# Kernel optimization log

Hardware: AMD Instinct MI355X
Metric: run time of the kernel (lower is better)

Reference implementation:

```python
import jax, jax.numpy as jnp
import numpy as np

N_NODES = 50000
N_EDGES = 800000
IN_CH = 128
HEADS = 4
OUT_CH = 32


def setup_inputs() -> dict:
    key = jax.random.key(0)
    k1, k2, k3, k4 = jax.random.split(key, 4)
    x = jax.random.normal(k1, (N_NODES, IN_CH), dtype=jnp.float32)
    edge_index = jax.random.randint(k2, (2, N_EDGES), 0, N_NODES, dtype=jnp.int64)
    # nn.Linear weight [out, in] with xavier-uniform init
    limW = float(np.sqrt(6.0 / (IN_CH + HEADS * OUT_CH)))
    W = jax.random.uniform(k3, (HEADS * OUT_CH, IN_CH), minval=-limW, maxval=limW, dtype=jnp.float32)
    lima = float(np.sqrt(6.0 / (HEADS + 2 * OUT_CH)))
    att = jax.random.uniform(k4, (HEADS, 2 * OUT_CH), minval=-lima, maxval=lima, dtype=jnp.float32)
    bias = jnp.zeros((HEADS * OUT_CH,), dtype=jnp.float32)
    return {"x": x, "edge_index": edge_index, "W": W, "att": att, "bias": bias}


def reference(x, edge_index, W, att, bias):
    n = x.shape[0]
    heads, two_c = att.shape
    out_ch = two_c // 2
    loop = jnp.arange(n, dtype=edge_index.dtype)
    src = jnp.concatenate([edge_index[0], loop])  # [E+n]
    dst = jnp.concatenate([edge_index[1], loop])  # [E+n]
    h = (x @ W.T).reshape(n, heads, out_ch)       # [n, H, C]
    h_src = h[src]                                # [E+n, H, C]
    h_dst = h[dst]                                # [E+n, H, C]
    # e = sum over channels of att applied to [h_src || h_dst]
    e = (jnp.einsum('ehc,hc->eh', h_src, att[:, :out_ch])
         + jnp.einsum('ehc,hc->eh', h_dst, att[:, out_ch:]))  # [E+n, H]
    e = jax.nn.leaky_relu(e, negative_slope=0.2)
    # segment softmax over incoming edges per dst node
    e_max = jax.ops.segment_max(e, dst, num_segments=n)        # [n, H]
    alpha = jnp.exp(e - e_max[dst])                            # [E+n, H]
    a_sum = jax.ops.segment_sum(alpha, dst, num_segments=n)    # [n, H]
    alpha = alpha / jnp.maximum(a_sum[dst], 1e-10)
    weighted = h_src * alpha[..., None]                        # [E+n, H, C]
    out = jax.ops.segment_sum(weighted, dst, num_segments=n)   # [n, H, C]
    out = out.reshape(n, heads * out_ch)                       # concat=True
    return out + bias
```

## Files before the change

### kernel.cpp

```cpp
#include <hip/hip_runtime.h>
#include <hip/hip_bf16.h>
#include <math.h>

#define N_NODES 50000
#define N_EDGES 800000
#define IN_CH   128
#define HEADS   4
#define OUT_CH  32
#define HC      128
#define WROWS   136

#define CB_SHIFT 7
#define CB_NODES 128
#define N_CB     391
#define NBK      128
#define EPB      (N_EDGES / NBK)
#define PCAP     44
#define ND_CAP   48
#define CB_CAP   2560

#define NG_TOT   782
#define NG_A     586
#define NG_B     (NG_TOT - NG_A)

typedef __attribute__((ext_vector_type(8))) short short8;
typedef __attribute__((ext_vector_type(4))) float floatx4;

__device__ __forceinline__ short f2bf(float f) {
    __hip_bfloat16 h = __float2bfloat16(f);
    return *reinterpret_cast<short*>(&h);
}

__device__ __forceinline__ void gemm_role(
    short* __restrict__ Wlds, int node_base,
    const float* __restrict__ x, const float* __restrict__ W,
    const float* __restrict__ att, __hip_bfloat16* __restrict__ hbuf,
    float* __restrict__ asrc, float* __restrict__ adst) {

    const int tid  = threadIdx.x;
    const int wave = tid >> 6;
    const int lane = tid & 63;
    const int col  = lane & 15;
    const int q    = lane >> 4;

    {
        int row  = tid >> 1;
        int half = tid & 1;
        const float4* Wr = (const float4*)(W + row * IN_CH + half * 64);
        short* dp = Wlds + row * WROWS + half * 64;
#pragma unroll
        for (int i = 0; i < 16; ++i) {
            float4 v = Wr[i];
            ushort4 p;
            p.x = (unsigned short)f2bf(v.x);
            p.y = (unsigned short)f2bf(v.y);
            p.z = (unsigned short)f2bf(v.z);
            p.w = (unsigned short)f2bf(v.w);
            *(ushort4*)(dp + i * 4) = p;
        }
    }

    float attS[8], attD[8];
#pragma unroll
    for (int t = 0; t < 8; ++t) {
        int base = (t >> 1) * 64 + (t & 1) * 16 + col;
        attS[t] = att[base];
        attD[t] = att[base + 32];
    }

    __syncthreads();

    const int node0 = node_base + wave * 16;
    const int m  = node0 + col;
    const int mc = min(m, N_NODES - 1);

    floatx4 acc[8];
#pragma unroll
    for (int t = 0; t < 8; ++t) acc[t] = (floatx4){0.f, 0.f, 0.f, 0.f};

#pragma unroll
    for (int ks = 0; ks < 4; ++ks) {
        const float4* xp = (const float4*)(x + (size_t)mc * IN_CH + ks * 32 + q * 8);
        float4 v0 = xp[0];
        float4 v1 = xp[1];
        short8 af;
        af[0] = f2bf(v0.x); af[1] = f2bf(v0.y); af[2] = f2bf(v0.z); af[3] = f2bf(v0.w);
        af[4] = f2bf(v1.x); af[5] = f2bf(v1.y); af[6] = f2bf(v1.z); af[7] = f2bf(v1.w);
#pragma unroll
        for (int t = 0; t < 8; ++t) {
            const short8 bf = *(const short8*)(Wlds + (t * 16 + col) * WROWS + ks * 32 + q * 8);
            acc[t] = __builtin_amdgcn_mfma_f32_16x16x32_bf16(af, bf, acc[t], 0, 0, 0);
        }
    }

#pragma unroll
    for (int r = 0; r < 4; ++r) {
        const int node = node0 + q * 4 + r;
        const bool valid = node < N_NODES;
        float hs[4] = {0.f, 0.f, 0.f, 0.f};
        float hd[4] = {0.f, 0.f, 0.f, 0.f};
#pragma unroll
        for (int t = 0; t < 8; ++t) {
            float v = acc[t][r];
            if (valid) hbuf[(size_t)node * HC + t * 16 + col] = __float2bfloat16(v);
            hs[t >> 1] = fmaf(v, attS[t], hs[t >> 1]);
            hd[t >> 1] = fmaf(v, attD[t], hd[t >> 1]);
        }
#pragma unroll
        for (int off = 8; off; off >>= 1) {
#pragma unroll
            for (int h = 0; h < 4; ++h) {
                hs[h] += __shfl_down(hs[h], off, 16);
                hd[h] += __shfl_down(hd[h], off, 16);
            }
        }
        if (col == 0 && valid) {
#pragma unroll
            for (int h = 0; h < 4; ++h) {
                asrc[node * HEADS + h] = hs[h];
                adst[node * HEADS + h] = hd[h];
            }
        }
    }
}

__global__ __launch_bounds__(256) void kA_fused(
    const int* __restrict__ src, const int* __restrict__ dst,
    unsigned* __restrict__ priv, int* __restrict__ cnt2,
    const float* __restrict__ x, const float* __restrict__ W,
    const float* __restrict__ att, __hip_bfloat16* __restrict__ hbuf,
    float* __restrict__ asrc, float* __restrict__ adst) {

    __shared__ short smem[128 * WROWS];
    const int tid = threadIdx.x;

    if (blockIdx.x < NBK) {
        int* lcnt = (int*)smem;
        const int blk = blockIdx.x;
        for (int i = tid; i < N_CB; i += 256) lcnt[i] = 0;
        __syncthreads();

        const int e0 = blk * EPB;
        for (int e = e0 + tid; e < e0 + EPB; e += 256) {
            int s = src[e];
            int d = dst[e];
            int cb = d >> CB_SHIFT;
            int pos = atomicAdd(&lcnt[cb], 1);
            if (pos < PCAP)
                priv[((size_t)cb * NBK + blk) * PCAP + pos] =
                    ((unsigned)(d & (CB_NODES - 1)) << 16) | (unsigned)s;
        }
        __syncthreads();
        for (int i = tid; i < N_CB; i += 256)
            cnt2[blk * N_CB + i] = min(lcnt[i], PCAP);
        return;
    }

    gemm_role(smem, (blockIdx.x - NBK) * 64, x, W, att, hbuf, asrc, adst);
}

__global__ __launch_bounds__(256) void kB_fused(
    const int* __restrict__ cnt2, const unsigned* __restrict__ priv,
    unsigned short* __restrict__ csr16, unsigned* __restrict__ meta,
    const float* __restrict__ x, const float* __restrict__ W,
    const float* __restrict__ att, __hip_bfloat16* __restrict__ hbuf,
    float* __restrict__ asrc, float* __restrict__ adst) {

    __shared__ short smem[128 * WROWS];
    const int tid = threadIdx.x;

    if (blockIdx.x >= N_CB) {
        gemm_role(smem, (NG_A + (int)blockIdx.x - N_CB) * 64, x, W, att, hbuf, asrc, adst);
        return;
    }

    unsigned short* list = (unsigned short*)smem;
    int* lcnt  = (int*)(smem + 6400);
    int* ccnt  = (int*)(smem + 6656);
    int* lpre  = (int*)(smem + 6912);
    int* lcnt2 = (int*)(smem + 7168);

    const int b = blockIdx.x;
    const int node0 = b << CB_SHIFT;
    const int nInB  = min(CB_NODES, N_NODES - node0);

    if (tid < CB_NODES) lcnt[tid] = 0;
    if (tid < NBK) lcnt2[tid] = cnt2[tid * N_CB + b];
    __syncthreads();

    const unsigned* p = priv + (size_t)b * NBK * PCAP;
    for (int idx = tid; idx < NBK * PCAP; idx += 256) {
        int blk = (idx * 5958) >> 18;
        int j   = idx - blk * PCAP;
        if (j < lcnt2[blk]) {
            unsigned ent = p[idx];
            int dl   = ent >> 16;
            int slot = atomicAdd(&lcnt[dl], 1);
            if (slot < ND_CAP) list[dl * ND_CAP + slot] = (unsigned short)(ent & 0xFFFFu);
        }
    }
    __syncthreads();

    if (tid < CB_NODES) { ccnt[tid] = min(lcnt[tid], ND_CAP); lpre[tid] = ccnt[tid]; }
    __syncthreads();
    for (int d = 1; d < CB_NODES; d <<= 1) {
        int v = (tid >= d && tid < CB_NODES) ? lpre[tid - d] : 0;
        __syncthreads();
        if (tid < CB_NODES) lpre[tid] += v;
        __syncthreads();
    }

    if (tid < nInB) {
        int cnt  = ccnt[tid];
        int excl = lpre[tid] - cnt;
        meta[node0 + tid] = (unsigned)(b * CB_CAP + excl) | ((unsigned)cnt << 24);
    }

    const int total = lpre[CB_NODES - 1];
    __syncthreads();
    for (int idx = tid; idx < total; idx += 256) {
        int n = 0;
#pragma unroll
        for (int s = 64; s; s >>= 1)
            if (idx >= lpre[n + s - 1]) n += s;
        int j = idx - (lpre[n] - ccnt[n]);
        csr16[b * CB_CAP + idx] = list[n * ND_CAP + j];
    }
}

__device__ __forceinline__ float edge_w(float t) {
    t = fmaxf(t, 0.2f * t);
    return __expf(t);
}

__global__ __launch_bounds__(256) void kb6_agg(
    const unsigned* __restrict__ meta, const unsigned short* __restrict__ csr16,
    const unsigned* __restrict__ hb, const float* __restrict__ asrc,
    const float* __restrict__ adst, const float* __restrict__ bias,
    float* __restrict__ out) {

    const int node = __builtin_amdgcn_readfirstlane(blockIdx.x * 4 + (threadIdx.x >> 6));
    if (node >= N_NODES) return;
    const int lane = threadIdx.x & 63;
    const int h    = lane >> 4;

    const unsigned mt = meta[node];
    const int cnt = (int)(mt >> 24);
    const unsigned short* p = csr16 + (mt & 0xFFFFFFu);

    const float ad = adst[node * HEADS + h];

    unsigned us = hb[node * 64 + lane];
    float wS = edge_w(asrc[node * HEADS + h] + ad);
    float ds = wS;
    float ax = wS * __uint_as_float(us << 16);
    float ay = wS * __uint_as_float(us & 0xffff0000u);

    int e = 0;
    for (; e + 7 < cnt; e += 8) {
        int s0 = p[e],     s1 = p[e + 1], s2 = p[e + 2], s3 = p[e + 3];
        int s4 = p[e + 4], s5 = p[e + 5], s6 = p[e + 6], s7 = p[e + 7];
        unsigned u0 = hb[s0 * 64 + lane];
        unsigned u1 = hb[s1 * 64 + lane];
        unsigned u2 = hb[s2 * 64 + lane];
        unsigned u3 = hb[s3 * 64 + lane];
        unsigned u4 = hb[s4 * 64 + lane];
        unsigned u5 = hb[s5 * 64 + lane];
        unsigned u6 = hb[s6 * 64 + lane];
        unsigned u7 = hb[s7 * 64 + lane];
        float w0 = edge_w(asrc[s0 * HEADS + h] + ad);
        float w1 = edge_w(asrc[s1 * HEADS + h] + ad);
        float w2 = edge_w(asrc[s2 * HEADS + h] + ad);
        float w3 = edge_w(asrc[s3 * HEADS + h] + ad);
        float w4 = edge_w(asrc[s4 * HEADS + h] + ad);
        float w5 = edge_w(asrc[s5 * HEADS + h] + ad);
        float w6 = edge_w(asrc[s6 * HEADS + h] + ad);
        float w7 = edge_w(asrc[s7 * HEADS + h] + ad);
        ds += ((w0 + w1) + (w2 + w3)) + ((w4 + w5) + (w6 + w7));
        ax = fmaf(w0, __uint_as_float(u0 << 16), ax);
        ay = fmaf(w0, __uint_as_float(u0 & 0xffff0000u), ay);
        ax = fmaf(w1, __uint_as_float(u1 << 16), ax);
        ay = fmaf(w1, __uint_as_float(u1 & 0xffff0000u), ay);
        ax = fmaf(w2, __uint_as_float(u2 << 16), ax);
        ay = fmaf(w2, __uint_as_float(u2 & 0xffff0000u), ay);
        ax = fmaf(w3, __uint_as_float(u3 << 16), ax);
        ay = fmaf(w3, __uint_as_float(u3 & 0xffff0000u), ay);
        ax = fmaf(w4, __uint_as_float(u4 << 16), ax);
        ay = fmaf(w4, __uint_as_float(u4 & 0xffff0000u), ay);
        ax = fmaf(w5, __uint_as_float(u5 << 16), ax);
        ay = fmaf(w5, __uint_as_float(u5 & 0xffff0000u), ay);
        ax = fmaf(w6, __uint_as_float(u6 << 16), ax);
        ay = fmaf(w6, __uint_as_float(u6 & 0xffff0000u), ay);
        ax = fmaf(w7, __uint_as_float(u7 << 16), ax);
        ay = fmaf(w7, __uint_as_float(u7 & 0xffff0000u), ay);
    }
    for (; e + 3 < cnt; e += 4) {
        int s0 = p[e], s1 = p[e + 1], s2 = p[e + 2], s3 = p[e + 3];
        unsigned u0 = hb[s0 * 64 + lane];
        unsigned u1 = hb[s1 * 64 + lane];
        unsigned u2 = hb[s2 * 64 + lane];
        unsigned u3 = hb[s3 * 64 + lane];
        float w0 = edge_w(asrc[s0 * HEADS + h] + ad);
        float w1 = edge_w(asrc[s1 * HEADS + h] + ad);
        float w2 = edge_w(asrc[s2 * HEADS + h] + ad);
        float w3 = edge_w(asrc[s3 * HEADS + h] + ad);
        ds += (w0 + w1) + (w2 + w3);
        ax = fmaf(w0, __uint_as_float(u0 << 16), ax);
        ay = fmaf(w0, __uint_as_float(u0 & 0xffff0000u), ay);
        ax = fmaf(w1, __uint_as_float(u1 << 16), ax);
        ay = fmaf(w1, __uint_as_float(u1 & 0xffff0000u), ay);
        ax = fmaf(w2, __uint_as_float(u2 << 16), ax);
        ay = fmaf(w2, __uint_as_float(u2 & 0xffff0000u), ay);
        ax = fmaf(w3, __uint_as_float(u3 << 16), ax);
        ay = fmaf(w3, __uint_as_float(u3 & 0xffff0000u), ay);
    }
    for (; e < cnt; ++e) {
        int s0 = p[e];
        unsigned u0 = hb[s0 * 64 + lane];
        float w0 = edge_w(asrc[s0 * HEADS + h] + ad);
        ds += w0;
        ax = fmaf(w0, __uint_as_float(u0 << 16), ax);
        ay = fmaf(w0, __uint_as_float(u0 & 0xffff0000u), ay);
    }

    float inv = 1.0f / fmaxf(ds, 1e-10f);
    float2 b = *(const float2*)(bias + lane * 2);
    float2 o;
    o.x = ax * inv + b.x;
    o.y = ay * inv + b.y;
    *(float2*)(out + (size_t)node * HC + lane * 2) = o;
}

extern "C" void kernel_launch(void* const* d_in, const int* in_sizes, int n_in,
                              void* d_out, int out_size, void* d_ws, size_t ws_size,
                              hipStream_t stream) {
    const float* x    = (const float*)d_in[0];
    const int*   ei   = (const int*)d_in[1];
    const float* W    = (const float*)d_in[2];
    const float* att  = (const float*)d_in[3];
    const float* bias = (const float*)d_in[4];
    float* out = (float*)d_out;

    const int* src = ei;
    const int* dst = ei + N_EDGES;

    char* ws = (char*)d_ws;
    __hip_bfloat16* hbuf = (__hip_bfloat16*)ws;
    float*    asrc = (float*)(ws + 12800000);
    float*    adst = (float*)(ws + 13600000);
    unsigned* priv = (unsigned*)(ws + 14400000);
    int*      cnt2 = (int*)(ws + 23208448);
    unsigned* meta = (unsigned*)(ws + 23408640);
    unsigned short* csr16 = (unsigned short*)(ws + 23608640);

    kA_fused<<<NBK + NG_A, 256, 0, stream>>>(src, dst, priv, cnt2,
                                             x, W, att, hbuf, asrc, adst);
    kB_fused<<<N_CB + NG_B, 256, 0, stream>>>(cnt2, priv, csr16, meta,
                                              x, W, att, hbuf, asrc, adst);
    kb6_agg<<<(N_NODES + 3) / 4, 256, 0, stream>>>(meta, csr16, (const unsigned*)hbuf,
                                                   asrc, adst, bias, out);
}
```

Baseline: 155.3 us.

## Fold attention vectors into GEMM weights and precompute bf16 weights once

Adds a one-block prep kernel that converts W to bf16 once and appends eight extra rows equal to W^T·att for the source and destination attention of each head. The GEMM then computes asrc/adst as a ninth MFMA tile, which removes the per-node shuffle reductions, and each GEMM block copies the prebuilt bf16 weights into LDS instead of converting them from fp32. The cost is an extra tiny serial kernel launch and attention logits that are now computed through bf16-rounded folded weights, which changes precision slightly.

```diff
diff --git a/kernel.cpp b/kernel.cpp
--- a/kernel.cpp
+++ b/kernel.cpp
@@ -31,23 +31,17 @@
     return *reinterpret_cast<short*>(&h);
 }
 
-__device__ __forceinline__ void gemm_role(
-    short* __restrict__ Wlds, int node_base,
-    const float* __restrict__ x, const float* __restrict__ W,
-    const float* __restrict__ att, __hip_bfloat16* __restrict__ hbuf,
-    float* __restrict__ asrc, float* __restrict__ adst) {
-
-    const int tid  = threadIdx.x;
-    const int wave = tid >> 6;
-    const int lane = tid & 63;
-    const int col  = lane & 15;
-    const int q    = lane >> 4;
+__global__ __launch_bounds__(256) void kP_prep(
+    const float* __restrict__ W, const float* __restrict__ att,
+    unsigned short* __restrict__ Wb) {
+
+    const int tid = threadIdx.x;
 
     {
         int row  = tid >> 1;
         int half = tid & 1;
         const float4* Wr = (const float4*)(W + row * IN_CH + half * 64);
-        short* dp = Wlds + row * WROWS + half * 64;
+        unsigned short* dp = Wb + row * WROWS + half * 64;
 #pragma unroll
         for (int i = 0; i < 16; ++i) {
             float4 v = Wr[i];
@@ -60,23 +54,49 @@
         }
     }
 
-    float attS[8], attD[8];
-#pragma unroll
-    for (int t = 0; t < 8; ++t) {
-        int base = (t >> 1) * 64 + (t & 1) * 16 + col;
-        attS[t] = att[base];
-        attD[t] = att[base + 32];
-    }
-
+#pragma unroll
+    for (int k = 0; k < 4; ++k) {
+        int idx  = tid + k * 256;
+        int j    = idx >> 7;
+        int i    = idx & 127;
+        int head = j & 3;
+        int aoff = (j & 4) ? 32 : 0;
+        float s = 0.f;
+#pragma unroll
+        for (int c = 0; c < 32; ++c)
+            s = fmaf(W[(head * 32 + c) * IN_CH + i], att[head * 64 + aoff + c], s);
+        Wb[(128 + j) * WROWS + i] = (unsigned short)f2bf(s);
+    }
+
+    for (int z = tid; z < 8 * WROWS; z += 256) Wb[136 * WROWS + z] = 0;
+}
+
+__device__ __forceinline__ void gemm_role(
+    short* __restrict__ Wlds, int node_base,
+    const float* __restrict__ x, const unsigned short* __restrict__ Wb,
+    __hip_bfloat16* __restrict__ hbuf,
+    float* __restrict__ asrc, float* __restrict__ adst) {
+
+    const int tid  = threadIdx.x;
+    const int wave = tid >> 6;
+    const int lane = tid & 63;
+    const int col  = lane & 15;
+    const int q    = lane >> 4;
+
+#pragma unroll
+    for (int i = 0; i < 10; ++i) {
+        int off = ((i << 2) + wave) * 64 + lane;
+        ((float4*)Wlds)[off] = ((const float4*)Wb)[off];
+    }
     __syncthreads();
 
     const int node0 = node_base + wave * 16;
     const int m  = node0 + col;
     const int mc = min(m, N_NODES - 1);
 
-    floatx4 acc[8];
-#pragma unroll
-    for (int t = 0; t < 8; ++t) acc[t] = (floatx4){0.f, 0.f, 0.f, 0.f};
+    floatx4 acc[9];
+#pragma unroll
+    for (int t = 0; t < 9; ++t) acc[t] = (floatx4){0.f, 0.f, 0.f, 0.f};
 
 #pragma unroll
     for (int ks = 0; ks < 4; ++ks) {
@@ -87,7 +107,7 @@
         af[0] = f2bf(v0.x); af[1] = f2bf(v0.y); af[2] = f2bf(v0.z); af[3] = f2bf(v0.w);
         af[4] = f2bf(v1.x); af[5] = f2bf(v1.y); af[6] = f2bf(v1.z); af[7] = f2bf(v1.w);
 #pragma unroll
-        for (int t = 0; t < 8; ++t) {
+        for (int t = 0; t < 9; ++t) {
             const short8 bf = *(const short8*)(Wlds + (t * 16 + col) * WROWS + ks * 32 + q * 8);
             acc[t] = __builtin_amdgcn_mfma_f32_16x16x32_bf16(af, bf, acc[t], 0, 0, 0);
         }
@@ -96,46 +116,28 @@
 #pragma unroll
     for (int r = 0; r < 4; ++r) {
         const int node = node0 + q * 4 + r;
-        const bool valid = node < N_NODES;
-        float hs[4] = {0.f, 0.f, 0.f, 0.f};
-        float hd[4] = {0.f, 0.f, 0.f, 0.f};
-#pragma unroll
-        for (int t = 0; t < 8; ++t) {
-            float v = acc[t][r];
-            if (valid) hbuf[(size_t)node * HC + t * 16 + col] = __float2bfloat16(v);
-            hs[t >> 1] = fmaf(v, attS[t], hs[t >> 1]);
-            hd[t >> 1] = fmaf(v, attD[t], hd[t >> 1]);
-        }
-#pragma unroll
-        for (int off = 8; off; off >>= 1) {
-#pragma unroll
-            for (int h = 0; h < 4; ++h) {
-                hs[h] += __shfl_down(hs[h], off, 16);
-                hd[h] += __shfl_down(hd[h], off, 16);
-            }
-        }
-        if (col == 0 && valid) {
-#pragma unroll
-            for (int h = 0; h < 4; ++h) {
-                asrc[node * HEADS + h] = hs[h];
-                adst[node * HEADS + h] = hd[h];
-            }
-        }
+        if (node >= N_NODES) continue;
+#pragma unroll
+        for (int t = 0; t < 8; ++t)
+            hbuf[(size_t)node * HC + t * 16 + col] = __float2bfloat16(acc[t][r]);
+        float v8 = acc[8][r];
+        if (col < 4)      asrc[node * HEADS + col] = v8;
+        else if (col < 8) adst[node * HEADS + col - 4] = v8;
     }
 }
 
 __global__ __launch_bounds__(256) void kA_fused(
     const int* __restrict__ src, const int* __restrict__ dst,
     unsigned* __restrict__ priv, int* __restrict__ cnt2,
-    const float* __restrict__ x, const float* __restrict__ W,
-    const float* __restrict__ att, __hip_bfloat16* __restrict__ hbuf,
+    const float* __restrict__ x, const unsigned short* __restrict__ Wb,
+    __hip_bfloat16* __restrict__ hbuf,
     float* __restrict__ asrc, float* __restrict__ adst) {
 
-    __shared__ short smem[128 * WROWS];
+    __shared__ float4 smem4[2560];
     const int tid = threadIdx.x;
 
     if (blockIdx.x < NBK) {
-        int* lcnt = (int*)smem;
+        int* lcnt = (int*)smem4;
         const int blk = blockIdx.x;
         for (int i = tid; i < N_CB; i += 256) lcnt[i] = 0;
         __syncthreads();
@@ -156,29 +158,31 @@
         return;
     }
 
-    gemm_role(smem, (blockIdx.x - NBK) * 64, x, W, att, hbuf, asrc, adst);
+    gemm_role((short*)smem4, (blockIdx.x - NBK) * 64, x, Wb, hbuf, asrc, adst);
 }
 
 __global__ __launch_bounds__(256) void kB_fused(
     const int* __restrict__ cnt2, const unsigned* __restrict__ priv,
     unsigned short* __restrict__ csr16, unsigned* __restrict__ meta,
-    const float* __restrict__ x, const float* __restrict__ W,
-    const float* __restrict__ att, __hip_bfloat16* __restrict__ hbuf,
+    const float* __restrict__ x, const unsigned short* __restrict__ Wb,
+    __hip_bfloat16* __restrict__ hbuf,
     float* __restrict__ asrc, float* __restrict__ adst) {
 
-    __shared__ short smem[128 * WROWS];
+    __shared__ float4 smem4[2560];
     const int tid = threadIdx.x;
 
     if (blockIdx.x >= N_CB) {
-        gemm_role(smem, (NG_A + (int)blockIdx.x - N_CB) * 64, x, W, att, hbuf, asrc, adst);
+        gemm_role((short*)smem4, (NG_A + (int)blockIdx.x - N_CB) * 64,
+                  x, Wb, hbuf, asrc, adst);
         return;
     }
 
+    char* smem = (char*)smem4;
     unsigned short* list = (unsigned short*)smem;
-    int* lcnt  = (int*)(smem + 6400);
-    int* ccnt  = (int*)(smem + 6656);
-    int* lpre  = (int*)(smem + 6912);
-    int* lcnt2 = (int*)(smem + 7168);
+    int* lcnt  = (int*)(smem + 12800);
+    int* ccnt  = (int*)(smem + 13312);
+    int* lpre  = (int*)(smem + 13824);
+    int* lcnt2 = (int*)(smem + 14336);
 
     const int b = blockIdx.x;
     const int node0 = b << CB_SHIFT;
@@ -350,13 +354,15 @@
     float*    adst = (float*)(ws + 13600000);
     unsigned* priv = (unsigned*)(ws + 14400000);
     int*      cnt2 = (int*)(ws + 23208448);
-    unsigned* meta = (unsigned*)(ws + 23408640);
-    unsigned short* csr16 = (unsigned short*)(ws + 23608640);
-
+    unsigned short* Wb = (unsigned short*)(ws + 23408640);
+    unsigned* meta = (unsigned*)(ws + 23449600);
+    unsigned short* csr16 = (unsigned short*)(ws + 23649600);
+
+    kP_prep<<<1, 256, 0, stream>>>(W, att, Wb);
     kA_fused<<<NBK + NG_A, 256, 0, stream>>>(src, dst, priv, cnt2,
-                                             x, W, att, hbuf, asrc, adst);
+                                             x, Wb, hbuf, asrc, adst);
     kB_fused<<<N_CB + NG_B, 256, 0, stream>>>(cnt2, priv, csr16, meta,
-                                              x, W, att, hbuf, asrc, adst);
+                                              x, Wb, hbuf, asrc, adst);
     kb6_agg<<<(N_NODES + 3) / 4, 256, 0, stream>>>(meta, csr16, (const unsigned*)hbuf,
                                                    asrc, adst, bias, out);
 }
```

Measured after the change: 160.3 us. 1.03x slower.
